# Kernel optimization log

Measured on AMD Instinct MI355X. Metric: run time of the kernel, lower is better.

Reference implementation:

```python
import jax, jax.numpy as jnp
import numpy as np

B, T, I, H = 128, 2048, 256, 256


def setup_inputs() -> dict:
    key = jax.random.key(0)
    k1, k2, k3 = jax.random.split(key, 3)
    # xavier-uniform-like scale for weights
    s_x = float(np.sqrt(6.0 / (I + H)))
    s_h = float(np.sqrt(6.0 / (H + H)))
    return {
        "x": jax.random.normal(k1, (B, T, I), dtype=jnp.float32),
        "w_x": jax.random.uniform(k2, (I, H), jnp.float32, -s_x, s_x),
        "b_x": jnp.zeros((H,), jnp.float32),
        "w_h": jax.random.uniform(k3, (H, H), jnp.float32, -s_h, s_h),
        "b_h": jnp.zeros((H,), jnp.float32),
    }


def reference(x, w_x, b_x, w_h, b_h):
    # The original computes identical pre-activations for all four gates:
    # z = x_t @ w_x + b_x + h @ w_h + b_h; f=i=o=sigmoid(z), g=tanh(z).
    # Precompute the input projection for all timesteps in one GEMM.
    b, t, _ = x.shape
    h0 = jnp.zeros((b, w_h.shape[0]), x.dtype)
    c0 = jnp.zeros_like(h0)
    xproj = jnp.einsum('bti,ih->tbh', x, w_x) + b_x  # [T, B, H]

    def step(carry, xp_t):
        h, c = carry
        z = xp_t + h @ w_h + b_h
        s = jax.nn.sigmoid(z)   # f_t == i_t == o_t
        g = jnp.tanh(z)         # g_t
        c_new = s * c + s * g
        h_new = s * jnp.tanh(c_new)
        return (h_new, c_new), None

    (h_t, c_t), _ = jax.lax.scan(step, (h0, c0), xproj)
    return (h_t, c_t)
```

## Files before the change

### kernel.cpp

```cpp
#include <hip/hip_runtime.h>
#include <stdint.h>

#define B_ 128
#define T_ 2048
#define I_ 256
#define H_ 256


__device__ __forceinline__ void gates_sg(float z, float& s, float& g){
  float az = fabsf(z);
  float a  = __expf(-az);
  float r1 = __builtin_amdgcn_rcpf(1.0f + a);
  s = (z >= 0.0f) ? r1 : a * r1;
  float a2 = a * a;
  float gm = (1.0f - a2) * __builtin_amdgcn_rcpf(1.0f + a2);
  g = (z >= 0.0f) ? gm : -gm;
}
__device__ __forceinline__ float tanh_stable(float c){
  float ac = fabsf(c);
  float u  = __expf(-2.0f * ac);
  float tm = (1.0f - u) * __builtin_amdgcn_rcpf(1.0f + u);
  return (c >= 0.0f) ? tm : -tm;
}

#define FMA4(hs, wv, ax, ay, az, aw)            \
  ax = fmaf(hs, wv.x, ax); ay = fmaf(hs, wv.y, ay); \
  az = fmaf(hs, wv.z, az); aw = fmaf(hs, wv.w, aw);


__global__ __launch_bounds__(512, 2) void xproj_k(
    const float* __restrict__ x, const float* __restrict__ w_x,
    const float* __restrict__ b_x, const float* __restrict__ b_h,
    float* __restrict__ xp, int t0c, int Tc)
{
  const int tid  = threadIdx.x;
  const int wv   = tid >> 6;
  const int lane = tid & 63;
  const int ks   = wv * 32;

  float4 w4[32];
  #pragma unroll
  for (int kk = 0; kk < 32; ++kk)
    w4[kk] = *(const float4*)&w_x[(ks + kk) * H_ + 4 * lane];

  float bias = 0.0f;
  if (tid < 256) bias = b_x[tid] + b_h[tid];

  __shared__ float4 xs4[256];
  __shared__ float  pb[8][4][256];

  const int rows_per_b = Tc >> 2;
  const int nblk = (B_ * Tc) >> 2;
  for (int bid = blockIdx.x; bid < nblk; bid += gridDim.x){
    const int b  = bid / rows_per_b;
    const int t4 = (bid - b * rows_per_b) << 2;
    __syncthreads();
    if (tid < 256)
      xs4[tid] = ((const float4*)x)[ (int64_t)(b * T_ + t0c + t4) * 64 + tid ];
    __syncthreads();
    #pragma unroll
    for (int rr = 0; rr < 4; ++rr){
      const float4* xr = &xs4[rr * 64 + (ks >> 2)];
      float ax = 0.f, ay = 0.f, az = 0.f, aw = 0.f;
      #pragma unroll
      for (int q = 0; q < 8; ++q){
        float4 hv = xr[q];
        FMA4(hv.x, w4[4*q+0], ax, ay, az, aw);
        FMA4(hv.y, w4[4*q+1], ax, ay, az, aw);
        FMA4(hv.z, w4[4*q+2], ax, ay, az, aw);
        FMA4(hv.w, w4[4*q+3], ax, ay, az, aw);
      }
      *(float4*)&pb[wv][rr][4*lane] = make_float4(ax, ay, az, aw);
    }
    __syncthreads();
    if (tid < 256){
      float z0 = bias, z1 = bias, z2 = bias, z3 = bias;
      #pragma unroll
      for (int w = 0; w < 8; ++w){
        z0 += pb[w][0][tid]; z1 += pb[w][1][tid];
        z2 += pb[w][2][tid]; z3 += pb[w][3][tid];
      }
      *(float4*)&xp[ ((int64_t)b * H_ + tid) * Tc + t4 ] = make_float4(z0, z1, z2, z3);
    }
  }
}


__global__ __launch_bounds__(512, 2) void rec_k(
    const float* __restrict__ xp, const float* __restrict__ w_h,
    float* __restrict__ out, int Tc, int init)
{
  const int tid  = threadIdx.x;
  const int wv   = tid >> 6;
  const int lane = tid & 63;
  const int ks   = wv * 32;
  const int b    = blockIdx.x;

  float4 w4[32];
  #pragma unroll
  for (int kk = 0; kk < 32; ++kk)
    w4[kk] = *(const float4*)&w_h[(ks + kk) * H_ + 4 * lane];

  __shared__ float hb[2][H_];
  __shared__ float pbuf[8][H_];

  float c = 0.f, hn = 0.f;
  const float* xpr = nullptr;
  float4 xq = make_float4(0,0,0,0), xq_next = make_float4(0,0,0,0);
  if (tid < 256){
    float h0 = init ? 0.f : out[(int64_t)b * H_ + tid];
    hb[0][tid] = h0;
    hn = h0;
    c  = init ? 0.f : out[(int64_t)B_ * H_ + (int64_t)b * H_ + tid];
    xpr = xp + ((int64_t)b * H_ + tid) * Tc;
    xq_next = *(const float4*)xpr;
  }
  __syncthreads();
  int p = 0;
  for (int t = 0; t < Tc; t += 4){
    if (tid < 256){
      xq = xq_next;
      if (t + 4 < Tc) xq_next = *(const float4*)(xpr + t + 4);
    }
    #pragma unroll
    for (int tt = 0; tt < 4; ++tt){
      const float4* hr = (const float4*)&hb[p][ks];
      float ax = 0.f, ay = 0.f, az = 0.f, aw = 0.f;
      #pragma unroll
      for (int q = 0; q < 8; ++q){
        float4 hv = hr[q];
        FMA4(hv.x, w4[4*q+0], ax, ay, az, aw);
        FMA4(hv.y, w4[4*q+1], ax, ay, az, aw);
        FMA4(hv.z, w4[4*q+2], ax, ay, az, aw);
        FMA4(hv.w, w4[4*q+3], ax, ay, az, aw);
      }
      *(float4*)&pbuf[wv][4*lane] = make_float4(ax, ay, az, aw);
      __syncthreads();
      if (tid < 256){
        float z = ((pbuf[0][tid] + pbuf[1][tid]) + (pbuf[2][tid] + pbuf[3][tid]))
                + ((pbuf[4][tid] + pbuf[5][tid]) + (pbuf[6][tid] + pbuf[7][tid]));
        z += (tt == 0) ? xq.x : (tt == 1) ? xq.y : (tt == 2) ? xq.z : xq.w;
        float s, g; gates_sg(z, s, g);
        c  = s * (c + g);
        hn = s * tanh_stable(c);
        hb[p ^ 1][tid] = hn;
      }
      __syncthreads();
      p ^= 1;
    }
  }
  if (tid < 256){
    out[(int64_t)b * H_ + tid] = hn;
    out[(int64_t)B_ * H_ + (int64_t)b * H_ + tid] = c;
  }
}


__global__ __launch_bounds__(512, 2) void lstm_fused_k(
    const float* __restrict__ x, const float* __restrict__ w_x,
    const float* __restrict__ b_x, const float* __restrict__ w_h,
    const float* __restrict__ b_h, float* __restrict__ out)
{
  const int tid  = threadIdx.x;
  const int wv   = tid >> 6;
  const int lane = tid & 63;
  const int ks   = wv * 32;
  const int b    = blockIdx.x;

  float4 wh4[32], wx4[32];
  #pragma unroll
  for (int kk = 0; kk < 32; ++kk){
    wh4[kk] = *(const float4*)&w_h[(ks + kk) * H_ + 4 * lane];
    wx4[kk] = *(const float4*)&w_x[(ks + kk) * H_ + 4 * lane];
  }
  float bias = 0.0f;
  if (tid < 256) bias = b_x[tid] + b_h[tid];

  __shared__ float hb[2][H_];
  __shared__ float4 xs4[2][64];
  const float* xrow = x + (int64_t)b * T_ * I_;
  if (tid < 256) hb[0][tid] = 0.f;
  if (tid < 64)  xs4[0][tid] = ((const float4*)xrow)[tid];
  __syncthreads();
  float c = 0.f, hn = 0.f;
  int p = 0;
  for (int t = 0; t < T_; ++t){
    const float4* hr = (const float4*)&hb[p][ks];
    const float4* xr = &xs4[p][ks >> 2];
    float ax = 0.f, ay = 0.f, az = 0.f, aw = 0.f;
    #pragma unroll
    for (int q = 0; q < 8; ++q){
      float4 hv = hr[q];
      FMA4(hv.x, wh4[4*q+0], ax, ay, az, aw);
      FMA4(hv.y, wh4[4*q+1], ax, ay, az, aw);
      FMA4(hv.z, wh4[4*q+2], ax, ay, az, aw);
      FMA4(hv.w, wh4[4*q+3], ax, ay, az, aw);
    }
    #pragma unroll
    for (int q = 0; q < 8; ++q){
      float4 xv = xr[q];
      FMA4(xv.x, wx4[4*q+0], ax, ay, az, aw);
      FMA4(xv.y, wx4[4*q+1], ax, ay, az, aw);
      FMA4(xv.z, wx4[4*q+2], ax, ay, az, aw);
      FMA4(xv.w, wx4[4*q+3], ax, ay, az, aw);
    }
    __shared__ float pbuf[8][H_];
    *(float4*)&pbuf[wv][4*lane] = make_float4(ax, ay, az, aw);
    __syncthreads();
    if (tid < 256){
      float z = bias
              + ((pbuf[0][tid] + pbuf[1][tid]) + (pbuf[2][tid] + pbuf[3][tid]))
              + ((pbuf[4][tid] + pbuf[5][tid]) + (pbuf[6][tid] + pbuf[7][tid]));
      float s, g; gates_sg(z, s, g);
      c  = s * (c + g);
      hn = s * tanh_stable(c);
      hb[p ^ 1][tid] = hn;
    } else if (tid < 320 && t + 1 < T_){
      xs4[p ^ 1][tid - 256] = ((const float4*)(xrow + (int64_t)(t + 1) * I_))[tid - 256];
    }
    __syncthreads();
    p ^= 1;
  }
  if (tid < 256){
    out[(int64_t)b * H_ + tid] = hn;
    out[(int64_t)B_ * H_ + (int64_t)b * H_ + tid] = c;
  }
}


extern "C" void kernel_launch(void* const* d_in, const int* in_sizes, int n_in,
                              void* d_out, int out_size, void* d_ws, size_t ws_size,
                              hipStream_t stream)
{
  const float* x   = (const float*)d_in[0];
  const float* w_x = (const float*)d_in[1];
  const float* b_x = (const float*)d_in[2];
  const float* w_h = (const float*)d_in[3];
  const float* b_h = (const float*)d_in[4];
  float* out = (float*)d_out;

  const size_t per_t = (size_t)B_ * H_ * sizeof(float);
  int Tc_max = (int)((ws_size / per_t) & ~(size_t)3);
  if (Tc_max >= 4){
    if (Tc_max > T_) Tc_max = T_;
    int done = 0, first = 1;
    while (done < T_){
      int Tc = (T_ - done < Tc_max) ? (T_ - done) : Tc_max;
      xproj_k<<<256, 512, 0, stream>>>(x, w_x, b_x, b_h, (float*)d_ws, done, Tc);
      rec_k<<<128, 512, 0, stream>>>((const float*)d_ws, w_h, out, Tc, first);
      done += Tc; first = 0;
    }
  } else {
    lstm_fused_k<<<128, 512, 0, stream>>>(x, w_x, b_x, w_h, b_h, out);
  }
}
```

Before: 2.248 ms.

## Cut recurrent step to one barrier via wave-local h ownership and double-buffered partials

The recurrence kernel now has each wave's first 32 lanes own the hidden columns that the same wave later reads as its K-slice. The h buffer can therefore be updated in place without a second block-wide barrier. Partial sums are double-buffered so one __syncthreads per timestep is enough, and the gate math is spread across all eight waves instead of four. The xproj kernel is changed to give each block a contiguous range of rows and to prefetch the next x row into registers while the current one is computed. This relies on ordering within a wave for LDS correctness and makes the synchronisation reasoning more subtle.

```diff
diff --git a/kernel.cpp b/kernel.cpp
--- a/kernel.cpp
+++ b/kernel.cpp
@@ -50,30 +50,48 @@
   __shared__ float  pb[8][4][256];
 
   const int rows_per_b = Tc >> 2;
-  const int nblk = (B_ * Tc) >> 2;
-  for (int bid = blockIdx.x; bid < nblk; bid += gridDim.x){
-    const int b  = bid / rows_per_b;
-    const int t4 = (bid - b * rows_per_b) << 2;
-    __syncthreads();
-    if (tid < 256)
-      xs4[tid] = ((const float4*)x)[ (int64_t)(b * T_ + t0c + t4) * 64 + tid ];
-    __syncthreads();
-    #pragma unroll
-    for (int rr = 0; rr < 4; ++rr){
-      const float4* xr = &xs4[rr * 64 + (ks >> 2)];
-      float ax = 0.f, ay = 0.f, az = 0.f, aw = 0.f;
+  const int nblk  = (B_ * Tc) >> 2;
+  const int iters = (nblk + gridDim.x - 1) / gridDim.x;
+  const int bid0  = blockIdx.x * iters;
+
+  float4 r = make_float4(0,0,0,0);
+  if (tid < 256 && bid0 < nblk){
+    const int b  = bid0 / rows_per_b;
+    const int t4 = (bid0 - b * rows_per_b) << 2;
+    r = ((const float4*)x)[ (int64_t)(b * T_ + t0c + t4) * 64 + tid ];
+  }
+
+  for (int i = 0; i < iters; ++i){
+    const int bid = bid0 + i;
+    const bool valid = bid < nblk;
+    if (tid < 256 && valid) xs4[tid] = r;
+    __syncthreads();
+    if (tid < 256 && bid + 1 < nblk){
+      const int bn = bid + 1;
+      const int b  = bn / rows_per_b;
+      const int t4 = (bn - b * rows_per_b) << 2;
+      r = ((const float4*)x)[ (int64_t)(b * T_ + t0c + t4) * 64 + tid ];
+    }
+    if (valid){
       #pragma unroll
-      for (int q = 0; q < 8; ++q){
-        float4 hv = xr[q];
-        FMA4(hv.x, w4[4*q+0], ax, ay, az, aw);
-        FMA4(hv.y, w4[4*q+1], ax, ay, az, aw);
-        FMA4(hv.z, w4[4*q+2], ax, ay, az, aw);
-        FMA4(hv.w, w4[4*q+3], ax, ay, az, aw);
-      }
-      *(float4*)&pb[wv][rr][4*lane] = make_float4(ax, ay, az, aw);
-    }
-    __syncthreads();
-    if (tid < 256){
+      for (int rr = 0; rr < 4; ++rr){
+        const float4* xr = &xs4[rr * 64 + (ks >> 2)];
+        float ax = 0.f, ay = 0.f, az = 0.f, aw = 0.f;
+        #pragma unroll
+        for (int q = 0; q < 8; ++q){
+          float4 hv = xr[q];
+          FMA4(hv.x, w4[4*q+0], ax, ay, az, aw);
+          FMA4(hv.y, w4[4*q+1], ax, ay, az, aw);
+          FMA4(hv.z, w4[4*q+2], ax, ay, az, aw);
+          FMA4(hv.w, w4[4*q+3], ax, ay, az, aw);
+        }
+        *(float4*)&pb[wv][rr][4*lane] = make_float4(ax, ay, az, aw);
+      }
+    }
+    __syncthreads();
+    if (valid && tid < 256){
+      const int b  = bid / rows_per_b;
+      const int t4 = (bid - b * rows_per_b) << 2;
       float z0 = bias, z1 = bias, z2 = bias, z3 = bias;
       #pragma unroll
       for (int w = 0; w < 8; ++w){
@@ -101,30 +119,33 @@
   for (int kk = 0; kk < 32; ++kk)
     w4[kk] = *(const float4*)&w_h[(ks + kk) * H_ + 4 * lane];
 
-  __shared__ float hb[2][H_];
-  __shared__ float pbuf[8][H_];
-
-  float c = 0.f, hn = 0.f;
-  const float* xpr = nullptr;
-  float4 xq = make_float4(0,0,0,0), xq_next = make_float4(0,0,0,0);
-  if (tid < 256){
-    float h0 = init ? 0.f : out[(int64_t)b * H_ + tid];
-    hb[0][tid] = h0;
-    hn = h0;
-    c  = init ? 0.f : out[(int64_t)B_ * H_ + (int64_t)b * H_ + tid];
-    xpr = xp + ((int64_t)b * H_ + tid) * Tc;
+  __shared__ float hb[H_];
+  __shared__ float pbuf[2][8][H_];
+
+  const int  col   = ks + (lane & 31);
+  const bool owner = (lane < 32);
+
+  float c = 0.f, hcur = 0.f;
+  const float* xpr = xp + ((int64_t)b * H_ + col) * Tc;
+  float xarr[4] = {0,0,0,0};
+  float4 xq_next = make_float4(0,0,0,0);
+  if (owner){
+    hcur = init ? 0.f : out[(int64_t)b * H_ + col];
+    c    = init ? 0.f : out[(int64_t)B_ * H_ + (int64_t)b * H_ + col];
+    hb[col] = hcur;
     xq_next = *(const float4*)xpr;
   }
   __syncthreads();
-  int p = 0;
+  int pp = 0;
   for (int t = 0; t < Tc; t += 4){
-    if (tid < 256){
-      xq = xq_next;
+    if (owner){
+      xarr[0] = xq_next.x; xarr[1] = xq_next.y;
+      xarr[2] = xq_next.z; xarr[3] = xq_next.w;
       if (t + 4 < Tc) xq_next = *(const float4*)(xpr + t + 4);
     }
     #pragma unroll
     for (int tt = 0; tt < 4; ++tt){
-      const float4* hr = (const float4*)&hb[p][ks];
+      const float4* hr = (const float4*)&hb[ks];
       float ax = 0.f, ay = 0.f, az = 0.f, aw = 0.f;
       #pragma unroll
       for (int q = 0; q < 8; ++q){
@@ -134,24 +155,26 @@
         FMA4(hv.z, w4[4*q+2], ax, ay, az, aw);
         FMA4(hv.w, w4[4*q+3], ax, ay, az, aw);
       }
-      *(float4*)&pbuf[wv][4*lane] = make_float4(ax, ay, az, aw);
+      *(float4*)&pbuf[pp][wv][4*lane] = make_float4(ax, ay, az, aw);
       __syncthreads();
-      if (tid < 256){
-        float z = ((pbuf[0][tid] + pbuf[1][tid]) + (pbuf[2][tid] + pbuf[3][tid]))
-                + ((pbuf[4][tid] + pbuf[5][tid]) + (pbuf[6][tid] + pbuf[7][tid]));
-        z += (tt == 0) ? xq.x : (tt == 1) ? xq.y : (tt == 2) ? xq.z : xq.w;
+      if (owner){
+        float z = xarr[tt];
+        float p0 = pbuf[pp][0][col], p1 = pbuf[pp][1][col];
+        float p2 = pbuf[pp][2][col], p3 = pbuf[pp][3][col];
+        float p4 = pbuf[pp][4][col], p5 = pbuf[pp][5][col];
+        float p6 = pbuf[pp][6][col], p7 = pbuf[pp][7][col];
+        z += ((p0 + p1) + (p2 + p3)) + ((p4 + p5) + (p6 + p7));
         float s, g; gates_sg(z, s, g);
-        c  = s * (c + g);
-        hn = s * tanh_stable(c);
-        hb[p ^ 1][tid] = hn;
-      }
-      __syncthreads();
-      p ^= 1;
-    }
-  }
-  if (tid < 256){
-    out[(int64_t)b * H_ + tid] = hn;
-    out[(int64_t)B_ * H_ + (int64_t)b * H_ + tid] = c;
+        c    = s * (c + g);
+        hcur = s * tanh_stable(c);
+        hb[col] = hcur;
+      }
+      pp ^= 1;
+    }
+  }
+  if (owner){
+    out[(int64_t)b * H_ + col] = hcur;
+    out[(int64_t)B_ * H_ + (int64_t)b * H_ + col] = c;
   }
 }
 
@@ -178,6 +201,7 @@
 
   __shared__ float hb[2][H_];
   __shared__ float4 xs4[2][64];
+  __shared__ float pbuf[8][H_];
   const float* xrow = x + (int64_t)b * T_ * I_;
   if (tid < 256) hb[0][tid] = 0.f;
   if (tid < 64)  xs4[0][tid] = ((const float4*)xrow)[tid];
@@ -204,7 +228,6 @@
       FMA4(xv.z, wx4[4*q+2], ax, ay, az, aw);
       FMA4(xv.w, wx4[4*q+3], ax, ay, az, aw);
     }
-    __shared__ float pbuf[8][H_];
     *(float4*)&pbuf[wv][4*lane] = make_float4(ax, ay, az, aw);
     __syncthreads();
     if (tid < 256){
```

Measured after the change: 2.211 ms. About the same (-1.6%).
